# Kernel tuning notes

Hardware: AMD Instinct MI355X
Metric: run time of the kernel (lower is better)

Reference implementation:

```python
import jax, jax.numpy as jnp
import numpy as np

WIN = 7
SHIFT = 3
HEADS = 6
EPS = 1e-5


def _rel_pos_index(ws):
    coords = np.stack(np.meshgrid(np.arange(ws), np.arange(ws), indexing='ij')).reshape(2, -1)
    rel = (coords[:, :, None] - coords[:, None, :]).transpose(1, 2, 0)  # (N, N, 2)
    rel[..., 0] += ws - 1
    rel[..., 1] += ws - 1
    rel[..., 0] *= 2 * ws - 1
    return jnp.asarray(rel.sum(-1).reshape(-1))  # (N*N,)


def _attn_mask(H, W, ws, ss):
    img = np.zeros((H, W))
    sl = (slice(0, -ws), slice(-ws, -ss), slice(-ss, None))
    cnt = 0
    for hs in sl:
        for wss in sl:
            img[hs, wss] = cnt
            cnt += 1
    mw = img.reshape(H // ws, ws, W // ws, ws).transpose(0, 2, 1, 3).reshape(-1, ws * ws)
    am = mw[:, None, :] - mw[:, :, None]  # (nw, N, N): mw[j]-mw[i]
    return jnp.asarray(np.where(am != 0, -1e9, 0.0).astype(np.float32))


def _layernorm(x, g, b):
    mu = x.mean(-1, keepdims=True)
    var = ((x - mu) ** 2).mean(-1, keepdims=True)
    return (x - mu) * jax.lax.rsqrt(var + EPS) * g + b


def setup_inputs() -> dict:
    key = jax.random.key(0)
    ks = jax.random.split(key, 6)
    B, H, W, C = 4, 224, 224, 192
    return {
        'x': jax.random.normal(ks[0], (B, H * W, C), jnp.float32),
        'norm1_g': jnp.ones((C,), jnp.float32),
        'norm1_b': jnp.zeros((C,), jnp.float32),
        'qkv_w': jax.random.normal(ks[1], (C, 3 * C), jnp.float32) * 0.02,
        'qkv_b': jnp.zeros((3 * C,), jnp.float32),
        'rpb_table': jax.random.normal(ks[2], ((2 * WIN - 1) ** 2, HEADS), jnp.float32) * 0.02,
        'proj_w': jax.random.normal(ks[3], (C, C), jnp.float32) * 0.02,
        'proj_b': jnp.zeros((C,), jnp.float32),
        'norm2_g': jnp.ones((C,), jnp.float32),
        'norm2_b': jnp.zeros((C,), jnp.float32),
        'fc1_w': jax.random.normal(ks[4], (C, 4 * C), jnp.float32) * 0.02,
        'fc1_b': jnp.zeros((4 * C,), jnp.float32),
        'fc2_w': jax.random.normal(ks[5], (4 * C, C), jnp.float32) * 0.02,
        'fc2_b': jnp.zeros((C,), jnp.float32),
        'h': 224,
        'w': 224,
    }


def reference(x, norm1_g, norm1_b, qkv_w, qkv_b, rpb_table, proj_w, proj_b,
              norm2_g, norm2_b, fc1_w, fc1_b, fc2_w, fc2_b, h, w):
    B, L, C = x.shape
    ch = C // HEADS
    N = WIN * WIN
    nh, nw = h // WIN, w // WIN
    rel_idx = _rel_pos_index(WIN)
    mask = _attn_mask(h, w, WIN, SHIFT)  # (nh*nw, N, N)

    shortcut = x
    xn = _layernorm(x, norm1_g, norm1_b).reshape(B, h, w, C)
    xs = jnp.roll(xn, (-SHIFT, -SHIFT), axis=(1, 2))
    # window partition -> (B*nh*nw, N, C)
    xw = xs.reshape(B, nh, WIN, nw, WIN, C).transpose(0, 1, 3, 2, 4, 5).reshape(B * nh * nw, N, C)

    qkv = (xw @ qkv_w + qkv_b).reshape(-1, N, 3, HEADS, ch).transpose(2, 0, 3, 1, 4)
    q, k, v = qkv[0], qkv[1], qkv[2]  # (NW, HEADS, N, ch)
    scale = ch ** -0.5
    attn = jnp.einsum('whic,whjc->whij', q * scale, k)
    bias = rpb_table[rel_idx].reshape(N, N, HEADS).transpose(2, 0, 1)  # (HEADS, N, N)
    attn = attn + bias[None]
    attn = attn.reshape(B, nh * nw, HEADS, N, N) + mask[None, :, None]
    attn = jax.nn.softmax(attn, axis=-1).reshape(B * nh * nw, HEADS, N, N)

    out = jnp.einsum('whij,whjc->whic', attn, v).transpose(0, 2, 1, 3).reshape(-1, N, C)
    out = out @ proj_w + proj_b
    # window reverse + roll back
    out = out.reshape(B, nh, nw, WIN, WIN, C).transpose(0, 1, 3, 2, 4, 5).reshape(B, h, w, C)
    out = jnp.roll(out, (SHIFT, SHIFT), axis=(1, 2)).reshape(B, L, C)

    x = shortcut + out
    xn2 = _layernorm(x, norm2_g, norm2_b)
    hid = jax.nn.gelu(xn2 @ fc1_w + fc1_b, approximate=False)
    return x + (hid @ fc2_w + fc2_b)
```

## Files before the change

kernel.cpp:

```cpp
#include <hip/hip_runtime.h>
#include <stdint.h>

#define MB    50176
#define CDIM  192

typedef __attribute__((ext_vector_type(8))) short bf16x8;
typedef __attribute__((ext_vector_type(4))) float f32x4;

#define WFENCE do{ asm volatile("s_waitcnt lgkmcnt(0)" ::: "memory"); \
                   __builtin_amdgcn_sched_barrier(0); }while(0)

__device__ __forceinline__ float wsum(float v){
  #pragma unroll
  for (int m=32;m>=1;m>>=1) v += __shfl_xor(v,m,64);
  return v;
}
__device__ __forceinline__ float bfbits2f(uint32_t h){
  union{uint32_t u; float f;} x; x.u = h<<16; return x.f;
}
__device__ __forceinline__ uint16_t f2bfbits(float f){
  union{float ff; uint32_t u;} x; x.ff = f;
  return (uint16_t)((x.u + 0x7FFFu + ((x.u>>16)&1u)) >> 16);
}
__device__ __forceinline__ void gload16(const void* g, void* l){
  __builtin_amdgcn_global_load_lds(
      (const __attribute__((address_space(1))) uint32_t*)g,
      (__attribute__((address_space(3))) uint32_t*)l, 16, 0, 0);
}
__device__ __forceinline__ size_t row2tok(int r_g){
  int widx = r_g/49, tpos = r_g - widx*49;
  int b = widx>>10, rem = widx&1023;
  int h = (rem>>5)*7 + tpos/7 + 3; if (h>=224) h-=224;
  int w = (rem&31)*7 + (tpos - (tpos/7)*7) + 3; if (w>=224) w-=224;
  return (size_t)b*MB + (size_t)h*224 + w;
}

__global__ __launch_bounds__(256) void prep_kernel(
    const float* __restrict__ qkv_w, const float* __restrict__ proj_w,
    const float* __restrict__ fc1_w, const float* __restrict__ fc2_w,
    const float* __restrict__ rpb,
    uint16_t* __restrict__ qkvW, uint16_t* __restrict__ prjW,
    uint16_t* __restrict__ fc1W, uint16_t* __restrict__ fc2W,
    float* __restrict__ btbl){
  int idx = blockIdx.x*256 + threadIdx.x;
  if (idx < 110592){ int k=idx/576, n=idx-k*576; qkvW[n*192+k]=f2bfbits(qkv_w[idx]); return; }
  idx -= 110592;
  if (idx < 36864){ int k=idx/192, n=idx-k*192; prjW[n*192+k]=f2bfbits(proj_w[idx]); return; }
  idx -= 36864;
  if (idx < 147456){ int k=idx/768, n=idx-k*768; fc1W[n*192+k]=f2bfbits(fc1_w[idx]); return; }
  idx -= 147456;
  if (idx < 147456){ int k=idx/192, n=idx-k*192; fc2W[n*768+k]=f2bfbits(fc2_w[idx]); return; }
  idx -= 147456;
  if (idx >= 98304) return;
  int j = idx & 63, i = (idx>>6) & 63;
  int hd = (idx>>12) % 6, cls = (idx>>12)/6;
  float v = -1e9f;
  if (i < 49 && j < 49){
    int dh = i/7 - j/7, dw = i%7 - j%7;
    v = rpb[((dh+6)*13 + (dw+6))*6 + hd];
    int cH = cls>>1, cW = cls&1;
    int li = (cH ? (i/7 < 4 ? 1 : 2) : 0)*3 + (cW ? (i%7 < 4 ? 1 : 2) : 0);
    int lj = (cH ? (j/7 < 4 ? 1 : 2) : 0)*3 + (cW ? (j%7 < 4 ? 1 : 2) : 0);
    if (li != lj) v = -1e9f;
  }
  btbl[idx] = v;
}

__global__ __launch_bounds__(256) void ln1_kernel(
    const float* __restrict__ x, const float* __restrict__ g,
    const float* __restrict__ bt, uint16_t* __restrict__ dst, int row0){
  int wid_l = (int)((blockIdx.x*256u + threadIdx.x) >> 6);
  int lane  = threadIdx.x & 63;
  size_t sidx = row2tok(row0 + wid_l);
  const float* s = x + sidx*CDIM;
  float v0=s[lane], v1=s[lane+64], v2=s[lane+128];
  float mu  = wsum(v0+v1+v2) * (1.f/192.f);
  float var = wsum(v0*v0+v1*v1+v2*v2)*(1.f/192.f) - mu*mu;
  float rs  = rsqrtf(var + 1e-5f);
  uint16_t* d = dst + (size_t)wid_l*CDIM;
  d[lane]     = f2bfbits((v0-mu)*rs*g[lane]     + bt[lane]);
  d[lane+64]  = f2bfbits((v1-mu)*rs*g[lane+64]  + bt[lane+64]);
  d[lane+128] = f2bfbits((v2-mu)*rs*g[lane+128] + bt[lane+128]);
}

enum { EPI_QKV=0, EPI_FC1=2, EPI_FC2=3 };

template<int EPI, int K, int NN>
__global__ __launch_bounds__(256) void mgemm(
    const uint16_t* __restrict__ A, const uint16_t* __restrict__ WT,
    const float* __restrict__ bias, void* __restrict__ outp,
    const float* __restrict__ resid, int row0){
  __shared__ __attribute__((aligned(16))) char As[256*128];
  __shared__ __attribute__((aligned(16))) char Bs[64*128];
  const int tid  = threadIdx.x;
  const int lane = tid & 63;
  const int wid  = tid >> 6;
  const int brow = blockIdx.y * 256;
  const int bcol = blockIdx.x * 64;
  const int srow = lane >> 3;
  const int sg   = (lane & 7) ^ srow;
  const int r16 = lane & 15, t4 = lane >> 4;

  f32x4 acc[4][4];
  #pragma unroll
  for (int m=0;m<4;m++)
    #pragma unroll
    for (int n=0;n<4;n++) acc[m][n] = (f32x4){0.f,0.f,0.f,0.f};

  for (int k0 = 0; k0 < K; k0 += 64){
    #pragma unroll
    for (int c = 0; c < 8; c++){
      int ch = wid*8 + c;
      gload16(A + (size_t)(brow + ch*8 + srow)*K + k0 + sg*8, As + ch*1024);
    }
    #pragma unroll
    for (int c = 0; c < 2; c++){
      int ch = wid*2 + c;
      gload16(WT + (size_t)(bcol + ch*8 + srow)*K + k0 + sg*8, Bs + ch*1024);
    }
    __syncthreads();

    bf16x8 af[4][2], bfr[4][2];
    #pragma unroll
    for (int m=0;m<4;m++)
      #pragma unroll
      for (int ks=0;ks<2;ks++){
        int arow = wid*64 + m*16 + r16;
        af[m][ks] = *(const bf16x8*)(As + arow*128 + (((ks*4+t4) ^ (arow&7))<<4));
      }
    #pragma unroll
    for (int n=0;n<4;n++)
      #pragma unroll
      for (int ks=0;ks<2;ks++){
        int brn = n*16 + r16;
        bfr[n][ks] = *(const bf16x8*)(Bs + brn*128 + (((ks*4+t4) ^ (brn&7))<<4));
      }
    #pragma unroll
    for (int m=0;m<4;m++)
      #pragma unroll
      for (int n=0;n<4;n++)
        #pragma unroll
        for (int ks=0;ks<2;ks++)
          acc[m][n] = __builtin_amdgcn_mfma_f32_16x16x32_bf16(
              af[m][ks], bfr[n][ks], acc[m][n], 0, 0, 0);
    __syncthreads();
  }

  float bi[4];
  #pragma unroll
  for (int n=0;n<4;n++) bi[n] = bias[bcol + n*16 + r16];
  #pragma unroll
  for (int m=0;m<4;m++){
    #pragma unroll
    for (int j=0;j<4;j++){
      int r = brow + wid*64 + m*16 + t4*4 + j;
      if constexpr (EPI==EPI_QKV || EPI==EPI_FC1){
        #pragma unroll
        for (int n=0;n<4;n++){
          float v = acc[m][n][j] + bi[n];
          if constexpr (EPI==EPI_FC1)
            v = 0.5f*v*(1.f + erff(v*0.70710678118654752f));
          ((uint16_t*)outp)[(size_t)r*NN + bcol + n*16 + r16] = f2bfbits(v);
        }
      } else {
        size_t pr = row2tok(row0 + r)*CDIM;
        #pragma unroll
        for (int n=0;n<4;n++){
          size_t p = pr + bcol + n*16 + r16;
          ((float*)outp)[p] = acc[m][n][j] + bi[n] + resid[p];
        }
      }
    }
  }
}

__global__ __launch_bounds__(384) void proj_ln2(
    const uint16_t* __restrict__ A, const uint16_t* __restrict__ WT,
    const float* __restrict__ pbias, const float* __restrict__ x,
    const float* __restrict__ g2, const float* __restrict__ b2,
    float* __restrict__ xout, uint16_t* __restrict__ ln2out, int row0){
  __shared__ __attribute__((aligned(16))) char As[128*128];
  __shared__ __attribute__((aligned(16))) char Bs[192*128];
  __shared__ float stats[3][128][2];
  const int tid  = threadIdx.x;
  const int lane = tid & 63;
  const int wid  = tid >> 6;
  const int pm = wid / 3, pn = wid - pm*3;
  const int brow = blockIdx.x * 128;
  const int srow = lane >> 3;
  const int sg   = (lane & 7) ^ srow;
  const int lrow16 = lane & 15, lkh = lane >> 4;

  f32x4 acc[4][4];
  #pragma unroll
  for (int m=0;m<4;m++)
    #pragma unroll
    for (int n=0;n<4;n++) acc[m][n] = (f32x4){0.f,0.f,0.f,0.f};

  for (int k0 = 0; k0 < 192; k0 += 64){
    for (int ch = wid; ch < 16; ch += 6)
      gload16(A + (size_t)(brow + ch*8 + srow)*192 + k0 + sg*8, As + ch*1024);
    for (int ch = wid; ch < 24; ch += 6)
      gload16(WT + (size_t)(ch*8 + srow)*192 + k0 + sg*8, Bs + ch*1024);
    __syncthreads();

    bf16x8 af[4][2], bfr[4][2];
    #pragma unroll
    for (int m=0;m<4;m++)
      #pragma unroll
      for (int ks=0;ks<2;ks++){
        int arow = pm*64 + m*16 + lrow16;
        af[m][ks] = *(const bf16x8*)(As + arow*128 + (((ks*4+lkh) ^ (arow&7))<<4));
      }
    #pragma unroll
    for (int n=0;n<4;n++)
      #pragma unroll
      for (int ks=0;ks<2;ks++){
        int brn = pn*64 + n*16 + lrow16;
        bfr[n][ks] = *(const bf16x8*)(Bs + brn*128 + (((ks*4+lkh) ^ (brn&7))<<4));
      }
    #pragma unroll
    for (int m=0;m<4;m++)
      #pragma unroll
      for (int n=0;n<4;n++)
        #pragma unroll
        for (int ks=0;ks<2;ks++)
          acc[m][n] = __builtin_amdgcn_mfma_f32_16x16x32_bf16(
              af[m][ks], bfr[n][ks], acc[m][n], 0, 0, 0);
    __syncthreads();
  }

  float bi[4], g2v[4], b2v[4];
  #pragma unroll
  for (int n=0;n<4;n++){
    int c = pn*64 + n*16 + lrow16;
    bi[n] = pbias[c]; g2v[n] = g2[c]; b2v[n] = b2[c];
  }
  #pragma unroll
  for (int m=0;m<4;m++){
    #pragma unroll
    for (int j=0;j<4;j++){
      int r = pm*64 + m*16 + lkh*4 + j;
      size_t pr = row2tok(row0 + brow + r)*CDIM;
      float s1 = 0.f, s2 = 0.f;
      #pragma unroll
      for (int n=0;n<4;n++){
        int c = pn*64 + n*16 + lrow16;
        float y = acc[m][n][j] + bi[n] + x[pr + c];
        acc[m][n][j] = y;
        xout[pr + c] = y;
        s1 += y; s2 = fmaf(y, y, s2);
      }
      #pragma unroll
      for (int mk=1; mk<16; mk<<=1){
        s1 += __shfl_xor(s1, mk, 64);
        s2 += __shfl_xor(s2, mk, 64);
      }
      if (lrow16 == 0){ stats[pn][r][0] = s1; stats[pn][r][1] = s2; }
    }
  }
  __syncthreads();
  #pragma unroll
  for (int m=0;m<4;m++){
    #pragma unroll
    for (int j=0;j<4;j++){
      int r = pm*64 + m*16 + lkh*4 + j;
      float s1 = stats[0][r][0] + stats[1][r][0] + stats[2][r][0];
      float s2 = stats[0][r][1] + stats[1][r][1] + stats[2][r][1];
      float mu = s1*(1.f/192.f);
      float rs = rsqrtf(s2*(1.f/192.f) - mu*mu + 1e-5f);
      size_t pr = (size_t)(brow + r)*CDIM;
      #pragma unroll
      for (int n=0;n<4;n++){
        int c = pn*64 + n*16 + lrow16;
        ln2out[pr + c] = f2bfbits((acc[m][n][j]-mu)*rs*g2v[n] + b2v[n]);
      }
    }
  }
}

__global__ __launch_bounds__(256) void attn_kernel(
    const uint16_t* __restrict__ qkv, const float* __restrict__ btbl,
    uint16_t* __restrict__ attnout, int win0){
  const int wv   = threadIdx.x >> 6;
  const int lane = threadIdx.x & 63;
  const int whd  = blockIdx.x*4 + wv;
  const int widx = whd/6, hd = whd - widx*6;
  const int r16 = lane & 15, t4 = lane >> 4;
  __shared__ uint16_t Vt[4][32][72];
  __shared__ uint16_t Pl[4][16][72];

  #pragma unroll
  for (int e=lane; e<32*16; e+=64){ Vt[wv][e>>4][48 + (e&15)] = 0; }
  for (int ch = lane; ch < 196; ch += 64){
    int j = ch >> 2, c0 = (ch&3)*8;
    const uint16_t* src = qkv + ((size_t)widx*49 + j)*576 + hd*32 + 384 + c0;
    uint4 v = *(const uint4*)src;
    uint32_t u[4] = {v.x, v.y, v.z, v.w};
    #pragma unroll
    for (int q=0;q<8;q++) Vt[wv][c0+q][j] = (uint16_t)(u[q>>1] >> ((q&1)*16));
  }

  bf16x8 kf[4];
  #pragma unroll
  for (int jt=0;jt<4;jt++)
    kf[jt] = *(const bf16x8*)(qkv + ((size_t)widx*49 + jt*16 + r16)*576 + hd*32 + 192 + t4*8);

  const int gw = win0 + widx;
  const int cls = ((((gw&1023)>>5)==31)<<1) | ((gw&31)==31);
  const float* tb = btbl + ((size_t)(cls*6 + hd) << 12);
  const float scale = 0.17677669529663689f;

  WFENCE;
  bf16x8 bv[2][2];
  #pragma unroll
  for (int ct=0;ct<2;ct++)
    #pragma unroll
    for (int ks=0;ks<2;ks++)
      bv[ct][ks] = *(const bf16x8*)&Vt[wv][ct*16 + r16][ks*32 + t4*8];

  #pragma unroll 1
  for (int it=0; it<4; it++){
    bf16x8 qf = *(const bf16x8*)(qkv + ((size_t)widx*49 + it*16 + r16)*576 + hd*32 + t4*8);
    f32x4 acc[4];
    #pragma unroll
    for (int jt=0;jt<4;jt++){
      acc[jt] = (f32x4){0.f,0.f,0.f,0.f};
      acc[jt] = __builtin_amdgcn_mfma_f32_16x16x32_bf16(kf[jt], qf, acc[jt], 0,0,0);
    }
    int i = it*16 + r16;
    float s[4][4];
    float m = -3.4e38f;
    #pragma unroll
    for (int jt=0;jt<4;jt++){
      float4 bvv = *(const float4*)(tb + i*64 + jt*16 + t4*4);
      float bb[4] = {bvv.x, bvv.y, bvv.z, bvv.w};
      #pragma unroll
      for (int r=0;r<4;r++){
        s[jt][r] = acc[jt][r]*scale + bb[r];
        m = fmaxf(m, s[jt][r]);
      }
    }
    m = fmaxf(m, __shfl_xor(m, 16, 64));
    m = fmaxf(m, __shfl_xor(m, 32, 64));
    float sum = 0.f;
    #pragma unroll
    for (int jt=0;jt<4;jt++)
      #pragma unroll
      for (int r=0;r<4;r++){
        s[jt][r] = __expf(s[jt][r] - m);
        sum += s[jt][r];
      }
    sum += __shfl_xor(sum, 16, 64);
    sum += __shfl_xor(sum, 32, 64);
    float inv = 1.f / sum;
    #pragma unroll
    for (int jt=0;jt<4;jt++){
      uint32_t lo = (uint32_t)f2bfbits(s[jt][0]*inv) | ((uint32_t)f2bfbits(s[jt][1]*inv) << 16);
      uint32_t hi = (uint32_t)f2bfbits(s[jt][2]*inv) | ((uint32_t)f2bfbits(s[jt][3]*inv) << 16);
      *(uint2*)&Pl[wv][r16][jt*16 + t4*4] = make_uint2(lo, hi);
    }
    WFENCE;

    f32x4 o[2];
    o[0] = (f32x4){0.f,0.f,0.f,0.f};
    o[1] = (f32x4){0.f,0.f,0.f,0.f};
    #pragma unroll
    for (int ks=0;ks<2;ks++){
      bf16x8 pa = *(const bf16x8*)&Pl[wv][r16][ks*32 + t4*8];
      #pragma unroll
      for (int ct=0;ct<2;ct++)
        o[ct] = __builtin_amdgcn_mfma_f32_16x16x32_bf16(pa, bv[ct][ks], o[ct], 0,0,0);
    }
    #pragma unroll
    for (int r=0;r<4;r++){
      int i2 = it*16 + t4*4 + r;
      if (i2 < 49){
        size_t base = ((size_t)widx*49 + i2)*CDIM + hd*32;
        attnout[base + r16]      = f2bfbits(o[0][r]);
        attnout[base + 16 + r16] = f2bfbits(o[1][r]);
      }
    }
  }
}

extern "C" void kernel_launch(void* const* d_in, const int* in_sizes, int n_in,
                              void* d_out, int out_size, void* d_ws, size_t ws_size,
                              hipStream_t stream) {
  const float* x       = (const float*)d_in[0];
  const float* n1g     = (const float*)d_in[1];
  const float* n1b     = (const float*)d_in[2];
  const float* qkv_w   = (const float*)d_in[3];
  const float* qkv_b   = (const float*)d_in[4];
  const float* rpb     = (const float*)d_in[5];
  const float* proj_w  = (const float*)d_in[6];
  const float* proj_b  = (const float*)d_in[7];
  const float* n2g     = (const float*)d_in[8];
  const float* n2b     = (const float*)d_in[9];
  const float* fc1_w   = (const float*)d_in[10];
  const float* fc1_b   = (const float*)d_in[11];
  const float* fc2_w   = (const float*)d_in[12];
  const float* fc2_b   = (const float*)d_in[13];
  float* out = (float*)d_out;

  const size_t TBL = 221184 + 73728 + 294912 + 294912 + 393216;
  size_t need_full = (size_t)200704*CDIM*2 + (size_t)200704*768*2 + TBL;
  bool full = ws_size >= need_full;
  int T  = full ? 200704 : MB;
  int NC = full ? 1 : 4;
  int NW = T / 49;

  char* ws = (char*)d_ws;
  uint16_t* Abuf = (uint16_t*)ws;
  uint16_t* Bq   = (uint16_t*)(ws + (size_t)T*CDIM*2);
  char* wbase    = ws + (size_t)T*CDIM*2 + (size_t)T*768*2;
  uint16_t* qkvW = (uint16_t*)wbase;
  uint16_t* prjW = (uint16_t*)(wbase + 221184);
  uint16_t* fc1W = (uint16_t*)(wbase + 221184 + 73728);
  uint16_t* fc2W = (uint16_t*)(wbase + 221184 + 73728 + 294912);
  float*    btbl = (float*)(wbase + 221184 + 73728 + 294912 + 294912);

  prep_kernel<<<2112, 256, 0, stream>>>(qkv_w, proj_w, fc1_w, fc2_w, rpb,
                                        qkvW, prjW, fc1W, fc2W, btbl);

  for (int c = 0; c < NC; c++){
    int row0 = c*T, win0 = row0/49;
    ln1_kernel<<<T/4, 256, 0, stream>>>(x, n1g, n1b, Abuf, row0);
    mgemm<EPI_QKV, 192, 576>
        <<<dim3(9, T/256), 256, 0, stream>>>(Abuf, qkvW, qkv_b, (void*)Bq, nullptr, 0);
    attn_kernel<<<NW*6/4, 256, 0, stream>>>(Bq, btbl, Abuf, win0);
    proj_ln2<<<T/128, 384, 0, stream>>>(Abuf, prjW, proj_b, x, n2g, n2b,
                                        out, Abuf, row0);
    mgemm<EPI_FC1, 192, 768>
        <<<dim3(12, T/256), 256, 0, stream>>>(Abuf, fc1W, fc1_b, (void*)Bq, nullptr, 0);
    mgemm<EPI_FC2, 768, 192>
        <<<dim3(3, T/256), 256, 0, stream>>>(Bq, fc2W, fc2_b, (void*)out, out, row0);
  }
}
```

Before: 860.2 us.

## Double-buffer GEMM tiles, shrink block tile, and halve intermediate buffer via two-pass chunking

The mgemm kernel moves from a 256x64 tile with a single LDS buffer to a 128x64 tile with double-buffered LDS. The next k-slice is prefetched while the current one is computed, with vmcnt waits and raw barriers in place of __syncthreads, and a 2x2 wave layout. The host path now splits the QKV/attention and FC1/FC2 stages into two halves, so the 768-wide intermediate buffer is half-sized and more likely to stay in cache. Smaller tiles mean more blocks but less reuse per block, and the extra launches add overhead.

```diff
diff --git a/kernel.cpp b/kernel.cpp
--- a/kernel.cpp
+++ b/kernel.cpp
@@ -90,83 +90,100 @@
     const uint16_t* __restrict__ A, const uint16_t* __restrict__ WT,
     const float* __restrict__ bias, void* __restrict__ outp,
     const float* __restrict__ resid, int row0){
-  __shared__ __attribute__((aligned(16))) char As[256*128];
-  __shared__ __attribute__((aligned(16))) char Bs[64*128];
+  __shared__ __attribute__((aligned(16))) char As[2][128*128];
+  __shared__ __attribute__((aligned(16))) char Bs[2][64*128];
   const int tid  = threadIdx.x;
   const int lane = tid & 63;
   const int wid  = tid >> 6;
-  const int brow = blockIdx.y * 256;
+  const int brow = blockIdx.y * 128;
   const int bcol = blockIdx.x * 64;
+
+  f32x4 acc[4][2];
+  #pragma unroll
+  for (int m=0;m<4;m++)
+    #pragma unroll
+    for (int n=0;n<2;n++) acc[m][n] = (f32x4){0.f,0.f,0.f,0.f};
+
   const int srow = lane >> 3;
   const int sg   = (lane & 7) ^ srow;
-  const int r16 = lane & 15, t4 = lane >> 4;
-
-  f32x4 acc[4][4];
-  #pragma unroll
-  for (int m=0;m<4;m++)
-    #pragma unroll
-    for (int n=0;n<4;n++) acc[m][n] = (f32x4){0.f,0.f,0.f,0.f};
-
-  for (int k0 = 0; k0 < K; k0 += 64){
-    #pragma unroll
-    for (int c = 0; c < 8; c++){
-      int ch = wid*8 + c;
-      gload16(A + (size_t)(brow + ch*8 + srow)*K + k0 + sg*8, As + ch*1024);
-    }
-    #pragma unroll
-    for (int c = 0; c < 2; c++){
-      int ch = wid*2 + c;
-      gload16(WT + (size_t)(bcol + ch*8 + srow)*K + k0 + sg*8, Bs + ch*1024);
-    }
-    __syncthreads();
-
-    bf16x8 af[4][2], bfr[4][2];
+  const int wm = wid >> 1, wn = wid & 1;
+  const int lrow16 = lane & 15, lkh = lane >> 4;
+
+  #define STAGE(k0, Ad, Bd) do{ \
+    _Pragma("unroll") \
+    for (int c = 0; c < 4; c++){ \
+      int ch = wid*4 + c; \
+      gload16(A + (size_t)(brow + ch*8 + srow)*K + (k0) + sg*8, (Ad) + ch*1024); \
+    } \
+    _Pragma("unroll") \
+    for (int c = 0; c < 2; c++){ \
+      int ch = wid*2 + c; \
+      gload16(WT + (size_t)(bcol + ch*8 + srow)*K + (k0) + sg*8, (Bd) + ch*1024); \
+    } \
+  }while(0)
+
+  constexpr int NK = K/64;
+  STAGE(0, As[0], Bs[0]);
+  #pragma unroll
+  for (int ki = 0; ki < NK; ki++){
+    const int cur = ki & 1;
+    if (ki+1 < NK){
+      STAGE((ki+1)*64, As[cur^1], Bs[cur^1]);
+      asm volatile("s_waitcnt vmcnt(6)" ::: "memory");
+    } else {
+      asm volatile("s_waitcnt vmcnt(0)" ::: "memory");
+    }
+    __builtin_amdgcn_s_barrier();
+    __builtin_amdgcn_sched_barrier(0);
+
+    bf16x8 af[4][2], bfr[2][2];
     #pragma unroll
     for (int m=0;m<4;m++)
       #pragma unroll
       for (int ks=0;ks<2;ks++){
-        int arow = wid*64 + m*16 + r16;
-        af[m][ks] = *(const bf16x8*)(As + arow*128 + (((ks*4+t4) ^ (arow&7))<<4));
-      }
-    #pragma unroll
-    for (int n=0;n<4;n++)
+        int arow = wm*64 + m*16 + lrow16;
+        af[m][ks] = *(const bf16x8*)(As[cur] + arow*128 + (((ks*4+lkh) ^ (arow&7))<<4));
+      }
+    #pragma unroll
+    for (int n=0;n<2;n++)
       #pragma unroll
       for (int ks=0;ks<2;ks++){
-        int brn = n*16 + r16;
-        bfr[n][ks] = *(const bf16x8*)(Bs + brn*128 + (((ks*4+t4) ^ (brn&7))<<4));
+        int brn = wn*32 + n*16 + lrow16;
+        bfr[n][ks] = *(const bf16x8*)(Bs[cur] + brn*128 + (((ks*4+lkh) ^ (brn&7))<<4));
       }
     #pragma unroll
     for (int m=0;m<4;m++)
       #pragma unroll
-      for (int n=0;n<4;n++)
+      for (int n=0;n<2;n++)
         #pragma unroll
         for (int ks=0;ks<2;ks++)
           acc[m][n] = __builtin_amdgcn_mfma_f32_16x16x32_bf16(
               af[m][ks], bfr[n][ks], acc[m][n], 0, 0, 0);
-    __syncthreads();
-  }
-
-  float bi[4];
-  #pragma unroll
-  for (int n=0;n<4;n++) bi[n] = bias[bcol + n*16 + r16];
+    if (ki+1 < NK) __builtin_amdgcn_s_barrier();
+  }
+  #undef STAGE
+
+  float bi[2];
+  #pragma unroll
+  for (int n=0;n<2;n++) bi[n] = bias[bcol + wn*32 + n*16 + lrow16];
   #pragma unroll
   for (int m=0;m<4;m++){
     #pragma unroll
     for (int j=0;j<4;j++){
-      int r = brow + wid*64 + m*16 + t4*4 + j;
+      int r = brow + wm*64 + m*16 + lkh*4 + j;
       if constexpr (EPI==EPI_QKV || EPI==EPI_FC1){
         #pragma unroll
-        for (int n=0;n<4;n++){
+        for (int n=0;n<2;n++){
           float v = acc[m][n][j] + bi[n];
           if constexpr (EPI==EPI_FC1)
             v = 0.5f*v*(1.f + erff(v*0.70710678118654752f));
-          ((uint16_t*)outp)[(size_t)r*NN + bcol + n*16 + r16] = f2bfbits(v);
+          ((uint16_t*)outp)[(size_t)r*NN + bcol + wn*32 + n*16 + lrow16] = f2bfbits(v);
         }
       } else {
         size_t pr = row2tok(row0 + r)*CDIM;
         #pragma unroll
-        for (int n=0;n<4;n++){
-          size_t p = pr + bcol + n*16 + r16;
+        for (int n=0;n<2;n++){
+          size_t p = pr + bcol + wn*32 + n*16 + lrow16;
           ((float*)outp)[p] = acc[m][n][j] + bi[n] + resid[p];
         }
       }
@@ -403,37 +420,67 @@
   const float* fc2_b   = (const float*)d_in[13];
   float* out = (float*)d_out;
 
+  const int T = 200704;
   const size_t TBL = 221184 + 73728 + 294912 + 294912 + 393216;
-  size_t need_full = (size_t)200704*CDIM*2 + (size_t)200704*768*2 + TBL;
+  size_t bq_bytes = (size_t)(T/2)*768*2;
+  size_t need_full = (size_t)T*CDIM*2 + bq_bytes + TBL;
   bool full = ws_size >= need_full;
-  int T  = full ? 200704 : MB;
-  int NC = full ? 1 : 4;
-  int NW = T / 49;
 
   char* ws = (char*)d_ws;
-  uint16_t* Abuf = (uint16_t*)ws;
-  uint16_t* Bq   = (uint16_t*)(ws + (size_t)T*CDIM*2);
-  char* wbase    = ws + (size_t)T*CDIM*2 + (size_t)T*768*2;
-  uint16_t* qkvW = (uint16_t*)wbase;
-  uint16_t* prjW = (uint16_t*)(wbase + 221184);
-  uint16_t* fc1W = (uint16_t*)(wbase + 221184 + 73728);
-  uint16_t* fc2W = (uint16_t*)(wbase + 221184 + 73728 + 294912);
-  float*    btbl = (float*)(wbase + 221184 + 73728 + 294912 + 294912);
-
-  prep_kernel<<<2112, 256, 0, stream>>>(qkv_w, proj_w, fc1_w, fc2_w, rpb,
-                                        qkvW, prjW, fc1W, fc2W, btbl);
-
-  for (int c = 0; c < NC; c++){
-    int row0 = c*T, win0 = row0/49;
-    ln1_kernel<<<T/4, 256, 0, stream>>>(x, n1g, n1b, Abuf, row0);
-    mgemm<EPI_QKV, 192, 576>
-        <<<dim3(9, T/256), 256, 0, stream>>>(Abuf, qkvW, qkv_b, (void*)Bq, nullptr, 0);
-    attn_kernel<<<NW*6/4, 256, 0, stream>>>(Bq, btbl, Abuf, win0);
+  if (full){
+    uint16_t* Abuf = (uint16_t*)ws;
+    uint16_t* Bq   = (uint16_t*)(ws + (size_t)T*CDIM*2);
+    char* wbase    = ws + (size_t)T*CDIM*2 + bq_bytes;
+    uint16_t* qkvW = (uint16_t*)wbase;
+    uint16_t* prjW = (uint16_t*)(wbase + 221184);
+    uint16_t* fc1W = (uint16_t*)(wbase + 221184 + 73728);
+    uint16_t* fc2W = (uint16_t*)(wbase + 221184 + 73728 + 294912);
+    float*    btbl = (float*)(wbase + 221184 + 73728 + 294912 + 294912);
+
+    prep_kernel<<<2112, 256, 0, stream>>>(qkv_w, proj_w, fc1_w, fc2_w, rpb,
+                                          qkvW, prjW, fc1W, fc2W, btbl);
+    const int H = T/2;
+    ln1_kernel<<<T/4, 256, 0, stream>>>(x, n1g, n1b, Abuf, 0);
+    for (int h=0; h<2; h++){
+      uint16_t* Ah = Abuf + (size_t)h*H*CDIM;
+      mgemm<EPI_QKV, 192, 576>
+          <<<dim3(9, H/128), 256, 0, stream>>>(Ah, qkvW, qkv_b, (void*)Bq, nullptr, 0);
+      attn_kernel<<<(H/49)*6/4, 256, 0, stream>>>(Bq, btbl, Ah, h*(H/49));
+    }
     proj_ln2<<<T/128, 384, 0, stream>>>(Abuf, prjW, proj_b, x, n2g, n2b,
-                                        out, Abuf, row0);
-    mgemm<EPI_FC1, 192, 768>
-        <<<dim3(12, T/256), 256, 0, stream>>>(Abuf, fc1W, fc1_b, (void*)Bq, nullptr, 0);
-    mgemm<EPI_FC2, 768, 192>
-        <<<dim3(3, T/256), 256, 0, stream>>>(Bq, fc2W, fc2_b, (void*)out, out, row0);
-  }
-}
+                                        out, Abuf, 0);
+    for (int h=0; h<2; h++){
+      uint16_t* Ah = Abuf + (size_t)h*H*CDIM;
+      mgemm<EPI_FC1, 192, 768>
+          <<<dim3(12, H/128), 256, 0, stream>>>(Ah, fc1W, fc1_b, (void*)Bq, nullptr, 0);
+      mgemm<EPI_FC2, 768, 192>
+          <<<dim3(3, H/128), 256, 0, stream>>>(Bq, fc2W, fc2_b, (void*)out, out, h*H);
+    }
+  } else {
+    const int TC = MB, NW = TC/49;
+    uint16_t* Abuf = (uint16_t*)ws;
+    uint16_t* Bq   = (uint16_t*)(ws + (size_t)TC*CDIM*2);
+    char* wbase    = ws + (size_t)TC*CDIM*2 + (size_t)TC*768*2;
+    uint16_t* qkvW = (uint16_t*)wbase;
+    uint16_t* prjW = (uint16_t*)(wbase + 221184);
+    uint16_t* fc1W = (uint16_t*)(wbase + 221184 + 73728);
+    uint16_t* fc2W = (uint16_t*)(wbase + 221184 + 73728 + 294912);
+    float*    btbl = (float*)(wbase + 221184 + 73728 + 294912 + 294912);
+
+    prep_kernel<<<2112, 256, 0, stream>>>(qkv_w, proj_w, fc1_w, fc2_w, rpb,
+                                          qkvW, prjW, fc1W, fc2W, btbl);
+    for (int c = 0; c < 4; c++){
+      int row0 = c*TC, win0 = row0/49;
+      ln1_kernel<<<TC/4, 256, 0, stream>>>(x, n1g, n1b, Abuf, row0);
+      mgemm<EPI_QKV, 192, 576>
+          <<<dim3(9, TC/128), 256, 0, stream>>>(Abuf, qkvW, qkv_b, (void*)Bq, nullptr, 0);
+      attn_kernel<<<NW*6/4, 256, 0, stream>>>(Bq, btbl, Abuf, win0);
+      proj_ln2<<<TC/128, 384, 0, stream>>>(Abuf, prjW, proj_b, x, n2g, n2b,
+                                           out, Abuf, row0);
+      mgemm<EPI_FC1, 192, 768>
+          <<<dim3(12, TC/128), 256, 0, stream>>>(Abuf, fc1W, fc1_b, (void*)Bq, nullptr, 0);
+      mgemm<EPI_FC2, 768, 192>
+          <<<dim3(3, TC/128), 256, 0, stream>>>(Bq, fc2W, fc2_b, (void*)out, out, row0);
+    }
+  }
+}
```

Measured after the change: 811.1 us. -5.7%, faster.
